# Kernel optimization log

Measured on AMD Instinct MI355X. Metric: run time of the kernel, lower is better.

## Reference

```python
import jax, jax.numpy as jnp
import numpy as np

B, S, C, H, W = 4, 8, 3, 384, 384
K = 5
CK = C * K


def conv1x1(x, w, b):
    # x: [B, Cin, H, W], w: [Cout, Cin], b: [Cout] -> [B, Cout, H, W]
    return jnp.einsum('bchw,oc->bohw', x, w) + b[None, :, None, None]


def mlp(x, w1, b1, w2, b2):
    return conv1x1(jax.nn.relu(conv1x1(x, w1, b1)), w2, b2)


def gaussian_density(x, mu_k, sigma):
    # x: [B,C,H,W], mu_k: [B,K,C,H,W], sigma: [B,K,H,W] -> density [B,K,H,W]
    s2 = sigma * sigma
    dist = jnp.sum((x[:, None] - mu_k) ** 2, axis=2)  # [B,K,H,W]
    return (2.0 * np.pi * s2) ** (-C / 2.0) * jnp.exp(-dist / (2.0 * s2))


def gmm_block(params, x, pi, mu, sigma):
    b = x.shape[0]
    mu_k = mu.reshape(b, K, C, H, W)
    dens = gaussian_density(x, mu_k, sigma)          # [B,K,H,W] (computed once, reused)
    alpha = pi * dens                                 # [B,K,H,W]
    rho = alpha * dens                                # [B,K,H,W]
    pi_new = jax.nn.softmax(mlp(jnp.concatenate([pi, alpha], 1), *params['pi']), axis=1)
    mu_new = jax.nn.sigmoid(mlp(jnp.concatenate([x, mu, rho], 1), *params['mu']))
    sigma_new = jnp.exp(jax.nn.relu(mlp(jnp.concatenate([x, mu_new, rho], 1), *params['sigma'])))
    dens2 = gaussian_density(x, mu_new.reshape(b, K, C, H, W), sigma_new)
    gamma = jax.nn.sigmoid(mlp(pi_new * dens2, *params['gamma']))  # [B,1,H,W]
    return pi_new, mu_new, sigma_new, gamma


def setup_inputs() -> dict:
    key = jax.random.key(0)
    ks = jax.random.split(key, 20)
    frames = jax.random.uniform(ks[0], (B, S, C, H, W), jnp.float32)
    targets = jax.random.uniform(ks[1], (B, S, C, H, W), jnp.float32)
    mu0 = jax.random.randint(ks[2], (B, CK, H, W), 0, 255).astype(jnp.float32) / 255.0
    def wb(k1, k2, cout, cin):
        return (jax.random.normal(k1, (cout, cin), jnp.float32) * 0.1,
                jax.random.normal(k2, (cout,), jnp.float32) * 0.1)
    pi_w1, pi_b1 = wb(ks[3], ks[4], K, 2 * K)
    pi_w2, pi_b2 = wb(ks[5], ks[6], K, K)
    mu_w1, mu_b1 = wb(ks[7], ks[8], CK, C + CK + K)
    mu_w2, mu_b2 = wb(ks[9], ks[10], CK, CK)
    sg_w1, sg_b1 = wb(ks[11], ks[12], K, C + CK + K)
    sg_w2, sg_b2 = wb(ks[13], ks[14], K, K)
    ga_w1, ga_b1 = wb(ks[15], ks[16], K, K)
    ga_w2, ga_b2 = wb(ks[17], ks[18], 1, K)
    return dict(frames=frames, targets=targets, mu0=mu0,
                pi_w1=pi_w1, pi_b1=pi_b1, pi_w2=pi_w2, pi_b2=pi_b2,
                mu_w1=mu_w1, mu_b1=mu_b1, mu_w2=mu_w2, mu_b2=mu_b2,
                sg_w1=sg_w1, sg_b1=sg_b1, sg_w2=sg_w2, sg_b2=sg_b2,
                ga_w1=ga_w1, ga_b1=ga_b1, ga_w2=ga_w2, ga_b2=ga_b2)


def reference(frames, targets, mu0,
              pi_w1, pi_b1, pi_w2, pi_b2,
              mu_w1, mu_b1, mu_w2, mu_b2,
              sg_w1, sg_b1, sg_w2, sg_b2,
              ga_w1, ga_b1, ga_w2, ga_b2):
    params = dict(pi=(pi_w1, pi_b1, pi_w2, pi_b2),
                  mu=(mu_w1, mu_b1, mu_w2, mu_b2),
                  sigma=(sg_w1, sg_b1, sg_w2, sg_b2),
                  gamma=(ga_w1, ga_b1, ga_w2, ga_b2))
    b = frames.shape[0]
    # init_gmm
    pi0 = jnp.ones((b, K, H, W), frames.dtype) / K
    sigma0 = jnp.ones((b, K, H, W), frames.dtype)

    def step(carry, frame):
        pi, mu, sigma = carry
        pi, mu, sigma, gamma = gmm_block(params, frame, pi, mu, sigma)
        return (pi, mu, sigma), gamma

    xs = jnp.moveaxis(frames, 1, 0)  # [S,B,C,H,W]
    _, gammas = jax.lax.scan(step, (pi0, mu0, sigma0), xs)
    return jnp.moveaxis(gammas, 0, 1)  # [B,S,1,H,W]
```

## Files before the change

### kernel.cpp

```cpp
#include <hip/hip_runtime.h>


namespace {

constexpr int Kk = 5;
constexpr int Cc = 3;
constexpr int CKc = 15;
constexpr int Bb = 4;
constexpr int Ss = 8;
constexpr int HWc = 384 * 384;
constexpr int BLOCK = 256;

constexpr int OPB1 = 0;
constexpr int OPW1 = 5;
constexpr int OPB2 = 55;
constexpr int OPW2 = 60;
constexpr int OMB1 = 85;
constexpr int OMW1 = 100;
constexpr int OMB2 = 445;
constexpr int OMW2 = 460;
constexpr int OSB1 = 685;
constexpr int OSW1 = 690;
constexpr int OSB2 = 805;
constexpr int OSW2 = 810;
constexpr int OGB1 = 835;
constexpr int OGW1 = 840;
constexpr int OGW2 = 865;
constexpr int OGB2 = 870;
constexpr int WTOT = 871;

__device__ __forceinline__ float rcpf(float x) { return __builtin_amdgcn_rcpf(x); }
__device__ __forceinline__ float ex2(float x) { return __builtin_amdgcn_exp2f(x); }
__device__ __forceinline__ float frelu(float a) { return fmaxf(a, 0.0f); }
constexpr float LOG2E = 1.4426950408889634f;
__device__ __forceinline__ float fsigm(float a) { return rcpf(1.0f + ex2(-LOG2E * a)); }

__global__ __launch_bounds__(256) void stage_ws_kernel(
    const float* __restrict__ pw1, const float* __restrict__ pb1,
    const float* __restrict__ pw2, const float* __restrict__ pb2,
    const float* __restrict__ mw1, const float* __restrict__ mb1,
    const float* __restrict__ mw2, const float* __restrict__ mb2,
    const float* __restrict__ sw1, const float* __restrict__ sb1,
    const float* __restrict__ sw2, const float* __restrict__ sb2,
    const float* __restrict__ gw1, const float* __restrict__ gb1,
    const float* __restrict__ gw2, const float* __restrict__ gb2,
    float* __restrict__ ws)
{
    const int t = threadIdx.x;
    auto cp = [&](const float* src, int off, int n) {
        for (int i = t; i < n; i += 256) ws[off + i] = src[i];
    };
    cp(pb1, OPB1, 5);   cp(pw1, OPW1, 50);
    cp(pb2, OPB2, 5);   cp(pw2, OPW2, 25);
    cp(mb1, OMB1, 15);  cp(mw1, OMW1, 345);
    cp(mb2, OMB2, 15);  cp(mw2, OMW2, 225);
    cp(sb1, OSB1, 5);   cp(sw1, OSW1, 115);
    cp(sb2, OSB2, 5);   cp(sw2, OSW2, 25);
    cp(gb1, OGB1, 5);   cp(gw1, OGW1, 25);
    cp(gw2, OGW2, 5);   cp(gb2, OGB2, 1);
}

__global__ __launch_bounds__(BLOCK, 4) void gmm_seq_kernel(
    const float* __restrict__ frames,
    const float* __restrict__ mu0,
    const float* __restrict__ Wt,
    float* __restrict__ out)
{
    const int t = blockIdx.x * BLOCK + threadIdx.x;
    const int b   = t / HWc;
    const int rem = t - b * HWc;

    const float C0 = 0.06349363593424097f;
    const float NH_L2E = -0.7213475204444817f;

    float pi[Kk], mu[CKc], rinv[Kk];
#pragma unroll
    for (int k = 0; k < Kk; k++) { pi[k] = 0.2f; rinv[k] = 1.0f; }
    {
        const float* mp = mu0 + (size_t)b * CKc * HWc;
#pragma unroll
        for (int j = 0; j < CKc; j++)
            mu[j] = mp[(size_t)j * HWc + rem];
    }

    const float* fbase = frames + ((size_t)b * Ss * Cc) * HWc;
    float x[Cc];
#pragma unroll
    for (int c = 0; c < Cc; c++)
        x[c] = fbase[(size_t)c * HWc + rem];

#pragma unroll 1
    for (int s = 0; s < Ss; s++) {
        long woff = 0;
        asm volatile("" : "+s"(woff));
        const float* W = Wt + woff;

        const int sn = (s + 1 < Ss) ? s + 1 : s;
        float xn[Cc];
        {
            const float* fp = fbase + ((size_t)sn * Cc) * HWc;
#pragma unroll
            for (int c = 0; c < Cc; c++)
                xn[c] = fp[(size_t)c * HWc + rem];
        }

        float alpha[Kk], rho[Kk];
#pragma unroll
        for (int k = 0; k < Kk; k++) {
            float inv_s2 = rinv[k] * rinv[k];
            float d0 = x[0] - mu[k * Cc + 0];
            float d1 = x[1] - mu[k * Cc + 1];
            float d2 = x[2] - mu[k * Cc + 2];
            float dist = fmaf(d0, d0, fmaf(d1, d1, d2 * d2));
            float coef = C0 * inv_s2 * rinv[k];
            float dens = coef * ex2(NH_L2E * dist * inv_s2);
            alpha[k] = pi[k] * dens;
            rho[k] = alpha[k] * dens;
        }

        float piN[Kk];
        {
            float h[Kk];
#pragma unroll
            for (int j = 0; j < Kk; j++) {
                float a = W[OPB1 + j];
#pragma unroll
                for (int i = 0; i < Kk; i++) a = fmaf(W[OPW1 + j * 2 * Kk + i], pi[i], a);
#pragma unroll
                for (int i = 0; i < Kk; i++) a = fmaf(W[OPW1 + j * 2 * Kk + Kk + i], alpha[i], a);
                h[j] = frelu(a);
            }
            float o[Kk];
            float m = -1e30f;
#pragma unroll
            for (int j = 0; j < Kk; j++) {
                float a = W[OPB2 + j];
#pragma unroll
                for (int i = 0; i < Kk; i++) a = fmaf(W[OPW2 + j * Kk + i], h[i], a);
                o[j] = a; m = fmaxf(m, a);
            }
            float sum = 0.0f;
#pragma unroll
            for (int j = 0; j < Kk; j++) { o[j] = ex2(LOG2E * (o[j] - m)); sum += o[j]; }
            float r = rcpf(sum);
#pragma unroll
            for (int j = 0; j < Kk; j++) piN[j] = o[j] * r;
        }

        float muN[CKc];
        {
            float h[CKc];
#pragma unroll
            for (int j = 0; j < CKc; j++) {
                float a = W[OMB1 + j];
#pragma unroll
                for (int i = 0; i < Cc; i++)  a = fmaf(W[OMW1 + j * 23 + i], x[i], a);
#pragma unroll
                for (int i = 0; i < CKc; i++) a = fmaf(W[OMW1 + j * 23 + 3 + i], mu[i], a);
#pragma unroll
                for (int i = 0; i < Kk; i++)  a = fmaf(W[OMW1 + j * 23 + 18 + i], rho[i], a);
                h[j] = frelu(a);
            }
#pragma unroll
            for (int j = 0; j < CKc; j++) {
                float a = W[OMB2 + j];
#pragma unroll
                for (int i = 0; i < CKc; i++) a = fmaf(W[OMW2 + j * CKc + i], h[i], a);
                muN[j] = fsigm(a);
            }
        }

        float rinvN[Kk];
        {
            float h[Kk];
#pragma unroll
            for (int j = 0; j < Kk; j++) {
                float a = W[OSB1 + j];
#pragma unroll
                for (int i = 0; i < Cc; i++)  a = fmaf(W[OSW1 + j * 23 + i], x[i], a);
#pragma unroll
                for (int i = 0; i < CKc; i++) a = fmaf(W[OSW1 + j * 23 + 3 + i], muN[i], a);
#pragma unroll
                for (int i = 0; i < Kk; i++)  a = fmaf(W[OSW1 + j * 23 + 18 + i], rho[i], a);
                h[j] = frelu(a);
            }
#pragma unroll
            for (int j = 0; j < Kk; j++) {
                float a = W[OSB2 + j];
#pragma unroll
                for (int i = 0; i < Kk; i++) a = fmaf(W[OSW2 + j * Kk + i], h[i], a);
                rinvN[j] = ex2(-LOG2E * frelu(a));
            }
        }

        float gin[Kk];
#pragma unroll
        for (int k = 0; k < Kk; k++) {
            float inv_s2 = rinvN[k] * rinvN[k];
            float d0 = x[0] - muN[k * Cc + 0];
            float d1 = x[1] - muN[k * Cc + 1];
            float d2 = x[2] - muN[k * Cc + 2];
            float dist = fmaf(d0, d0, fmaf(d1, d1, d2 * d2));
            float coef = C0 * inv_s2 * rinvN[k];
            gin[k] = piN[k] * (coef * ex2(NH_L2E * dist * inv_s2));
        }
        {
            float h[Kk];
#pragma unroll
            for (int j = 0; j < Kk; j++) {
                float a = W[OGB1 + j];
#pragma unroll
                for (int i = 0; i < Kk; i++) a = fmaf(W[OGW1 + j * Kk + i], gin[i], a);
                h[j] = frelu(a);
            }
            float go = W[OGB2];
#pragma unroll
            for (int i = 0; i < Kk; i++) go = fmaf(W[OGW2 + i], h[i], go);
            out[(size_t)(b * Ss + s) * HWc + rem] = fsigm(go);
        }

#pragma unroll
        for (int k = 0; k < Kk; k++) { pi[k] = piN[k]; rinv[k] = rinvN[k]; }
#pragma unroll
        for (int j = 0; j < CKc; j++) mu[j] = muN[j];
#pragma unroll
        for (int c = 0; c < Cc; c++) x[c] = xn[c];
    }
}

}

extern "C" void kernel_launch(void* const* d_in, const int* in_sizes, int n_in,
                              void* d_out, int out_size, void* d_ws, size_t ws_size,
                              hipStream_t stream) {
    const float* frames = (const float*)d_in[0];
    const float* mu0    = (const float*)d_in[2];
    const float* pw1 = (const float*)d_in[3];
    const float* pb1 = (const float*)d_in[4];
    const float* pw2 = (const float*)d_in[5];
    const float* pb2 = (const float*)d_in[6];
    const float* mw1 = (const float*)d_in[7];
    const float* mb1 = (const float*)d_in[8];
    const float* mw2 = (const float*)d_in[9];
    const float* mb2 = (const float*)d_in[10];
    const float* sw1 = (const float*)d_in[11];
    const float* sb1 = (const float*)d_in[12];
    const float* sw2 = (const float*)d_in[13];
    const float* sb2 = (const float*)d_in[14];
    const float* gw1 = (const float*)d_in[15];
    const float* gb1 = (const float*)d_in[16];
    const float* gw2 = (const float*)d_in[17];
    const float* gb2 = (const float*)d_in[18];
    float* out = (float*)d_out;
    float* ws  = (float*)d_ws;

    stage_ws_kernel<<<1, 256, 0, stream>>>(
        pw1, pb1, pw2, pb2, mw1, mb1, mw2, mb2,
        sw1, sb1, sw2, sb2, gw1, gb1, gw2, gb2, ws);

    const int total = Bb * HWc;
    const int grid = (total + BLOCK - 1) / BLOCK;

    gmm_seq_kernel<<<grid, BLOCK, 0, stream>>>(frames, mu0, ws, out);
}
```

Before: 302.5 us.

## Pack MLP outputs into float2 pairs for packed FMA on CDNA

```diff
diff --git a/kernel.cpp b/kernel.cpp
--- a/kernel.cpp
+++ b/kernel.cpp
@@ -3,37 +3,59 @@
 
 namespace {
 
-constexpr int Kk = 5;
 constexpr int Cc = 3;
-constexpr int CKc = 15;
 constexpr int Bb = 4;
 constexpr int Ss = 8;
 constexpr int HWc = 384 * 384;
 constexpr int BLOCK = 256;
 
 constexpr int OPB1 = 0;
-constexpr int OPW1 = 5;
-constexpr int OPB2 = 55;
-constexpr int OPW2 = 60;
-constexpr int OMB1 = 85;
-constexpr int OMW1 = 100;
-constexpr int OMB2 = 445;
-constexpr int OMW2 = 460;
-constexpr int OSB1 = 685;
-constexpr int OSW1 = 690;
-constexpr int OSB2 = 805;
-constexpr int OSW2 = 810;
-constexpr int OGB1 = 835;
-constexpr int OGW1 = 840;
-constexpr int OGW2 = 865;
-constexpr int OGB2 = 870;
-constexpr int WTOT = 871;
+constexpr int OPW1 = 6;
+constexpr int OPB2 = 66;
+constexpr int OPW2 = 72;
+constexpr int OMB1 = 102;
+constexpr int OMW1 = 118;
+constexpr int OMB2 = 486;
+constexpr int OMW2 = 504;
+constexpr int OSB1 = 774;
+constexpr int OSW1 = 780;
+constexpr int OSB2 = 918;
+constexpr int OSW2 = 924;
+constexpr int OGB1 = 954;
+constexpr int OGW1 = 960;
+constexpr int OGW2 = 990;
+constexpr int OGB2 = 995;
+constexpr int WTOT = 996;
+
+constexpr int HPB1 = OPB1 / 2;
+constexpr int HPW1 = OPW1 / 2;
+constexpr int HPB2 = OPB2 / 2;
+constexpr int HPW2 = OPW2 / 2;
+constexpr int HMB1 = OMB1 / 2;
+constexpr int HMW1 = OMW1 / 2;
+constexpr int HMB2 = OMB2 / 2;
+constexpr int HMW2 = OMW2 / 2;
+constexpr int HSB1 = OSB1 / 2;
+constexpr int HSW1 = OSW1 / 2;
+constexpr int HSB2 = OSB2 / 2;
+constexpr int HSW2 = OSW2 / 2;
+constexpr int HGB1 = OGB1 / 2;
+constexpr int HGW1 = OGW1 / 2;
+
+typedef float v2f __attribute__((ext_vector_type(2)));
 
 __device__ __forceinline__ float rcpf(float x) { return __builtin_amdgcn_rcpf(x); }
 __device__ __forceinline__ float ex2(float x) { return __builtin_amdgcn_exp2f(x); }
-__device__ __forceinline__ float frelu(float a) { return fmaxf(a, 0.0f); }
+
+__device__ __forceinline__ v2f vsplat(float w) { v2f r = {w, w}; return r; }
+__device__ __forceinline__ v2f vfma(v2f a, v2f b, v2f c) { return __builtin_elementwise_fma(a, b, c); }
+__device__ __forceinline__ v2f vexp2(v2f v) { v2f r; r.x = ex2(v.x); r.y = ex2(v.y); return r; }
+__device__ __forceinline__ v2f vrcp(v2f v) { v2f r; r.x = rcpf(v.x); r.y = rcpf(v.y); return r; }
+__device__ __forceinline__ v2f vmax(v2f a, v2f b) { return __builtin_elementwise_max(a, b); }
+__device__ __forceinline__ v2f vrelu(v2f a) { return vmax(a, vsplat(0.0f)); }
 constexpr float LOG2E = 1.4426950408889634f;
-__device__ __forceinline__ float fsigm(float a) { return rcpf(1.0f + ex2(-LOG2E * a)); }
+__device__ __forceinline__ v2f vsigm(v2f a) { return vrcp(vsplat(1.0f) + vexp2(vsplat(-LOG2E) * a)); }
+__device__ __forceinline__ float hx(v2f v, int sel) { return sel ? v.y : v.x; }
 
 __global__ __launch_bounds__(256) void stage_ws_kernel(
     const float* __restrict__ pw1, const float* __restrict__ pb1,
@@ -47,20 +69,34 @@
     float* __restrict__ ws)
 {
     const int t = threadIdx.x;
-    auto cp = [&](const float* src, int off, int n) {
-        for (int i = t; i < n; i += 256) ws[off + i] = src[i];
+    auto pairs = [&](const float* w, const float* bsrc, int I, int NP,
+                     const int* lo, const int* hi, int wOff, int bOff) {
+        for (int idx = t; idx < I * NP; idx += 256) {
+            int i = idx / NP, p = idx - (idx / NP) * NP;
+            ws[wOff + 2 * idx]     = w[lo[p] * I + i];
+            ws[wOff + 2 * idx + 1] = (hi[p] >= 0) ? w[hi[p] * I + i] : 0.0f;
+        }
+        for (int p = t; p < NP; p += 256) {
+            ws[bOff + 2 * p]     = bsrc[lo[p]];
+            ws[bOff + 2 * p + 1] = (hi[p] >= 0) ? bsrc[hi[p]] : 0.0f;
+        }
     };
-    cp(pb1, OPB1, 5);   cp(pw1, OPW1, 50);
-    cp(pb2, OPB2, 5);   cp(pw2, OPW2, 25);
-    cp(mb1, OMB1, 15);  cp(mw1, OMW1, 345);
-    cp(mb2, OMB2, 15);  cp(mw2, OMW2, 225);
-    cp(sb1, OSB1, 5);   cp(sw1, OSW1, 115);
-    cp(sb2, OSB2, 5);   cp(sw2, OSW2, 25);
-    cp(gb1, OGB1, 5);   cp(gw1, OGW1, 25);
-    cp(gw2, OGW2, 5);   cp(gb2, OGB2, 1);
+    const int lo3[3] = {0, 2, 4},                 hi3[3] = {1, 3, -1};
+    const int lo8[8] = {0, 2, 4, 6, 8, 10, 12, 14}, hi8[8] = {1, 3, 5, 7, 9, 11, 13, -1};
+    const int lo9[9] = {0, 1, 2, 6, 7, 8, 12, 13, 14}, hi9[9] = {3, 4, 5, 9, 10, 11, -1, -1, -1};
+    pairs(pw1, pb1, 10, 3, lo3, hi3, OPW1, OPB1);
+    pairs(pw2, pb2,  5, 3, lo3, hi3, OPW2, OPB2);
+    pairs(mw1, mb1, 23, 8, lo8, hi8, OMW1, OMB1);
+    pairs(mw2, mb2, 15, 9, lo9, hi9, OMW2, OMB2);
+    pairs(sw1, sb1, 23, 3, lo3, hi3, OSW1, OSB1);
+    pairs(sw2, sb2,  5, 3, lo3, hi3, OSW2, OSB2);
+    pairs(gw1, gb1,  5, 3, lo3, hi3, OGW1, OGB1);
+    if (t < 5)  ws[OGW2 + t] = gw2[t];
+    if (t == 0) ws[OGB2] = gb2[0];
 }
 
-__global__ __launch_bounds__(BLOCK, 4) void gmm_seq_kernel(
+__global__ __launch_bounds__(BLOCK, 4)
+void gmm_seq_kernel(
     const float* __restrict__ frames,
     const float* __restrict__ mu0,
     const float* __restrict__ Wt,
@@ -73,156 +109,205 @@
     const float C0 = 0.06349363593424097f;
     const float NH_L2E = -0.7213475204444817f;
 
-    float pi[Kk], mu[CKc], rinv[Kk];
-#pragma unroll
-    for (int k = 0; k < Kk; k++) { pi[k] = 0.2f; rinv[k] = 1.0f; }
+    v2f piP[3], muP[9], rinvP[3];
+    piP[0] = vsplat(0.2f); piP[1] = vsplat(0.2f); piP[2] = {0.2f, 0.0f};
+    rinvP[0] = vsplat(1.0f); rinvP[1] = vsplat(1.0f); rinvP[2] = {1.0f, 0.0f};
     {
-        const float* mp = mu0 + (size_t)b * CKc * HWc;
-#pragma unroll
-        for (int j = 0; j < CKc; j++)
-            mu[j] = mp[(size_t)j * HWc + rem];
+        const float* mp = mu0 + (size_t)b * 15 * HWc;
+#pragma unroll
+        for (int kp = 0; kp < 3; kp++)
+#pragma unroll
+            for (int c = 0; c < 3; c++) {
+                float lo = mp[(size_t)((2 * kp) * 3 + c) * HWc + rem];
+                float hi = (kp < 2) ? mp[(size_t)((2 * kp + 1) * 3 + c) * HWc + rem] : 0.0f;
+                muP[kp * 3 + c] = {lo, hi};
+            }
     }
 
     const float* fbase = frames + ((size_t)b * Ss * Cc) * HWc;
     float x[Cc];
 #pragma unroll
-    for (int c = 0; c < Cc; c++)
-        x[c] = fbase[(size_t)c * HWc + rem];
+    for (int c = 0; c < Cc; c++) x[c] = fbase[(size_t)c * HWc + rem];
 
 #pragma unroll 1
     for (int s = 0; s < Ss; s++) {
         long woff = 0;
         asm volatile("" : "+s"(woff));
         const float* W = Wt + woff;
+        const v2f* W2 = reinterpret_cast<const v2f*>(W);
 
         const int sn = (s + 1 < Ss) ? s + 1 : s;
         float xn[Cc];
         {
             const float* fp = fbase + ((size_t)sn * Cc) * HWc;
 #pragma unroll
-            for (int c = 0; c < Cc; c++)
-                xn[c] = fp[(size_t)c * HWc + rem];
-        }
-
-        float alpha[Kk], rho[Kk];
-#pragma unroll
-        for (int k = 0; k < Kk; k++) {
-            float inv_s2 = rinv[k] * rinv[k];
-            float d0 = x[0] - mu[k * Cc + 0];
-            float d1 = x[1] - mu[k * Cc + 1];
-            float d2 = x[2] - mu[k * Cc + 2];
-            float dist = fmaf(d0, d0, fmaf(d1, d1, d2 * d2));
-            float coef = C0 * inv_s2 * rinv[k];
-            float dens = coef * ex2(NH_L2E * dist * inv_s2);
-            alpha[k] = pi[k] * dens;
-            rho[k] = alpha[k] * dens;
-        }
-
-        float piN[Kk];
-        {
-            float h[Kk];
-#pragma unroll
-            for (int j = 0; j < Kk; j++) {
-                float a = W[OPB1 + j];
-#pragma unroll
-                for (int i = 0; i < Kk; i++) a = fmaf(W[OPW1 + j * 2 * Kk + i], pi[i], a);
-#pragma unroll
-                for (int i = 0; i < Kk; i++) a = fmaf(W[OPW1 + j * 2 * Kk + Kk + i], alpha[i], a);
-                h[j] = frelu(a);
-            }
-            float o[Kk];
-            float m = -1e30f;
-#pragma unroll
-            for (int j = 0; j < Kk; j++) {
-                float a = W[OPB2 + j];
-#pragma unroll
-                for (int i = 0; i < Kk; i++) a = fmaf(W[OPW2 + j * Kk + i], h[i], a);
-                o[j] = a; m = fmaxf(m, a);
-            }
-            float sum = 0.0f;
-#pragma unroll
-            for (int j = 0; j < Kk; j++) { o[j] = ex2(LOG2E * (o[j] - m)); sum += o[j]; }
+            for (int c = 0; c < Cc; c++) xn[c] = fp[(size_t)c * HWc + rem];
+        }
+
+        v2f xs[Cc];
+#pragma unroll
+        for (int c = 0; c < Cc; c++) xs[c] = vsplat(x[c]);
+
+        v2f alpha2[3], rho2[3];
+#pragma unroll
+        for (int kp = 0; kp < 3; kp++) {
+            v2f ri  = rinvP[kp];
+            v2f is2 = ri * ri;
+            v2f d0 = xs[0] - muP[kp * 3 + 0];
+            v2f d1 = xs[1] - muP[kp * 3 + 1];
+            v2f d2 = xs[2] - muP[kp * 3 + 2];
+            v2f dist = vfma(d0, d0, vfma(d1, d1, d2 * d2));
+            v2f coef = vsplat(C0) * is2 * ri;
+            v2f dens = coef * vexp2(vsplat(NH_L2E) * dist * is2);
+            alpha2[kp] = piP[kp] * dens;
+            rho2[kp]   = alpha2[kp] * dens;
+        }
+
+        {
+            v2f hp[3];
+#pragma unroll
+            for (int p = 0; p < 3; p++) hp[p] = W2[HPB1 + p];
+#pragma unroll
+            for (int i = 0; i < 5; i++) {
+                v2f sv = vsplat(hx(piP[i >> 1], i & 1));
+#pragma unroll
+                for (int p = 0; p < 3; p++) hp[p] = vfma(W2[HPW1 + i * 3 + p], sv, hp[p]);
+            }
+#pragma unroll
+            for (int i = 0; i < 5; i++) {
+                v2f sv = vsplat(hx(alpha2[i >> 1], i & 1));
+#pragma unroll
+                for (int p = 0; p < 3; p++) hp[p] = vfma(W2[HPW1 + (5 + i) * 3 + p], sv, hp[p]);
+            }
+#pragma unroll
+            for (int p = 0; p < 3; p++) hp[p] = vrelu(hp[p]);
+
+            v2f o2[3];
+#pragma unroll
+            for (int p = 0; p < 3; p++) o2[p] = W2[HPB2 + p];
+#pragma unroll
+            for (int i = 0; i < 5; i++) {
+                v2f sv = vsplat(hx(hp[i >> 1], i & 1));
+#pragma unroll
+                for (int p = 0; p < 3; p++) o2[p] = vfma(W2[HPW2 + i * 3 + p], sv, o2[p]);
+            }
+            float m = fmaxf(fmaxf(fmaxf(o2[0].x, o2[0].y), fmaxf(o2[1].x, o2[1].y)), o2[2].x);
+            v2f e0 = vexp2(vsplat(LOG2E) * (o2[0] - vsplat(m)));
+            v2f e1 = vexp2(vsplat(LOG2E) * (o2[1] - vsplat(m)));
+            v2f e2 = vexp2(vsplat(LOG2E) * (o2[2] - vsplat(m)));
+            float sum = e0.x + e0.y + e1.x + e1.y + e2.x;
             float r = rcpf(sum);
-#pragma unroll
-            for (int j = 0; j < Kk; j++) piN[j] = o[j] * r;
-        }
-
-        float muN[CKc];
-        {
-            float h[CKc];
-#pragma unroll
-            for (int j = 0; j < CKc; j++) {
-                float a = W[OMB1 + j];
-#pragma unroll
-                for (int i = 0; i < Cc; i++)  a = fmaf(W[OMW1 + j * 23 + i], x[i], a);
-#pragma unroll
-                for (int i = 0; i < CKc; i++) a = fmaf(W[OMW1 + j * 23 + 3 + i], mu[i], a);
-#pragma unroll
-                for (int i = 0; i < Kk; i++)  a = fmaf(W[OMW1 + j * 23 + 18 + i], rho[i], a);
-                h[j] = frelu(a);
-            }
-#pragma unroll
-            for (int j = 0; j < CKc; j++) {
-                float a = W[OMB2 + j];
-#pragma unroll
-                for (int i = 0; i < CKc; i++) a = fmaf(W[OMW2 + j * CKc + i], h[i], a);
-                muN[j] = fsigm(a);
-            }
-        }
-
-        float rinvN[Kk];
-        {
-            float h[Kk];
-#pragma unroll
-            for (int j = 0; j < Kk; j++) {
-                float a = W[OSB1 + j];
-#pragma unroll
-                for (int i = 0; i < Cc; i++)  a = fmaf(W[OSW1 + j * 23 + i], x[i], a);
-#pragma unroll
-                for (int i = 0; i < CKc; i++) a = fmaf(W[OSW1 + j * 23 + 3 + i], muN[i], a);
-#pragma unroll
-                for (int i = 0; i < Kk; i++)  a = fmaf(W[OSW1 + j * 23 + 18 + i], rho[i], a);
-                h[j] = frelu(a);
-            }
-#pragma unroll
-            for (int j = 0; j < Kk; j++) {
-                float a = W[OSB2 + j];
-#pragma unroll
-                for (int i = 0; i < Kk; i++) a = fmaf(W[OSW2 + j * Kk + i], h[i], a);
-                rinvN[j] = ex2(-LOG2E * frelu(a));
-            }
-        }
-
-        float gin[Kk];
-#pragma unroll
-        for (int k = 0; k < Kk; k++) {
-            float inv_s2 = rinvN[k] * rinvN[k];
-            float d0 = x[0] - muN[k * Cc + 0];
-            float d1 = x[1] - muN[k * Cc + 1];
-            float d2 = x[2] - muN[k * Cc + 2];
-            float dist = fmaf(d0, d0, fmaf(d1, d1, d2 * d2));
-            float coef = C0 * inv_s2 * rinvN[k];
-            gin[k] = piN[k] * (coef * ex2(NH_L2E * dist * inv_s2));
-        }
-        {
-            float h[Kk];
-#pragma unroll
-            for (int j = 0; j < Kk; j++) {
-                float a = W[OGB1 + j];
-#pragma unroll
-                for (int i = 0; i < Kk; i++) a = fmaf(W[OGW1 + j * Kk + i], gin[i], a);
-                h[j] = frelu(a);
-            }
+            piP[0] = e0 * vsplat(r); piP[1] = e1 * vsplat(r); piP[2] = e2 * vsplat(r);
+        }
+
+        {
+            v2f hm[8];
+#pragma unroll
+            for (int p = 0; p < 8; p++) hm[p] = W2[HMB1 + p];
+#pragma unroll
+            for (int c = 0; c < 3; c++) {
+#pragma unroll
+                for (int p = 0; p < 8; p++) hm[p] = vfma(W2[HMW1 + c * 8 + p], xs[c], hm[p]);
+            }
+#pragma unroll
+            for (int j = 0; j < 15; j++) {
+                const int k = j / 3, c = j - 3 * (j / 3);
+                v2f sv = vsplat(hx(muP[(k >> 1) * 3 + c], k & 1));
+#pragma unroll
+                for (int p = 0; p < 8; p++) hm[p] = vfma(W2[HMW1 + (3 + j) * 8 + p], sv, hm[p]);
+            }
+#pragma unroll
+            for (int k = 0; k < 5; k++) {
+                v2f sv = vsplat(hx(rho2[k >> 1], k & 1));
+#pragma unroll
+                for (int p = 0; p < 8; p++) hm[p] = vfma(W2[HMW1 + (18 + k) * 8 + p], sv, hm[p]);
+            }
+#pragma unroll
+            for (int p = 0; p < 8; p++) hm[p] = vrelu(hm[p]);
+
+            v2f am[9];
+#pragma unroll
+            for (int q = 0; q < 9; q++) am[q] = W2[HMB2 + q];
+#pragma unroll
+            for (int j = 0; j < 15; j++) {
+                v2f sv = vsplat(hx(hm[j >> 1], j & 1));
+#pragma unroll
+                for (int q = 0; q < 9; q++) am[q] = vfma(W2[HMW2 + j * 9 + q], sv, am[q]);
+            }
+#pragma unroll
+            for (int q = 0; q < 9; q++) muP[q] = vsigm(am[q]);
+        }
+
+        {
+            v2f hs[3];
+#pragma unroll
+            for (int p = 0; p < 3; p++) hs[p] = W2[HSB1 + p];
+#pragma unroll
+            for (int c = 0; c < 3; c++) {
+#pragma unroll
+                for (int p = 0; p < 3; p++) hs[p] = vfma(W2[HSW1 + c * 3 + p], xs[c], hs[p]);
+            }
+#pragma unroll
+            for (int j = 0; j < 15; j++) {
+                const int k = j / 3, c = j - 3 * (j / 3);
+                v2f sv = vsplat(hx(muP[(k >> 1) * 3 + c], k & 1));
+#pragma unroll
+                for (int p = 0; p < 3; p++) hs[p] = vfma(W2[HSW1 + (3 + j) * 3 + p], sv, hs[p]);
+            }
+#pragma unroll
+            for (int k = 0; k < 5; k++) {
+                v2f sv = vsplat(hx(rho2[k >> 1], k & 1));
+#pragma unroll
+                for (int p = 0; p < 3; p++) hs[p] = vfma(W2[HSW1 + (18 + k) * 3 + p], sv, hs[p]);
+            }
+#pragma unroll
+            for (int p = 0; p < 3; p++) hs[p] = vrelu(hs[p]);
+
+            v2f as2[3];
+#pragma unroll
+            for (int p = 0; p < 3; p++) as2[p] = W2[HSB2 + p];
+#pragma unroll
+            for (int i = 0; i < 5; i++) {
+                v2f sv = vsplat(hx(hs[i >> 1], i & 1));
+#pragma unroll
+                for (int p = 0; p < 3; p++) as2[p] = vfma(W2[HSW2 + i * 3 + p], sv, as2[p]);
+            }
+#pragma unroll
+            for (int p = 0; p < 3; p++)
+                rinvP[p] = vexp2(vsplat(-LOG2E) * vrelu(as2[p]));
+        }
+
+        v2f gin[3];
+#pragma unroll
+        for (int kp = 0; kp < 3; kp++) {
+            v2f ri  = rinvP[kp];
+            v2f is2 = ri * ri;
+            v2f d0 = xs[0] - muP[kp * 3 + 0];
+            v2f d1 = xs[1] - muP[kp * 3 + 1];
+            v2f d2 = xs[2] - muP[kp * 3 + 2];
+            v2f dist = vfma(d0, d0, vfma(d1, d1, d2 * d2));
+            v2f coef = vsplat(C0) * is2 * ri;
+            gin[kp] = piP[kp] * (coef * vexp2(vsplat(NH_L2E) * dist * is2));
+        }
+        {
+            v2f hg[3];
+#pragma unroll
+            for (int p = 0; p < 3; p++) hg[p] = W2[HGB1 + p];
+#pragma unroll
+            for (int i = 0; i < 5; i++) {
+                v2f sv = vsplat(hx(gin[i >> 1], i & 1));
+#pragma unroll
+                for (int p = 0; p < 3; p++) hg[p] = vfma(W2[HGW1 + i * 3 + p], sv, hg[p]);
+            }
+#pragma unroll
+            for (int p = 0; p < 3; p++) hg[p] = vrelu(hg[p]);
+
             float go = W[OGB2];
 #pragma unroll
-            for (int i = 0; i < Kk; i++) go = fmaf(W[OGW2 + i], h[i], go);
-            out[(size_t)(b * Ss + s) * HWc + rem] = fsigm(go);
-        }
-
-#pragma unroll
-        for (int k = 0; k < Kk; k++) { pi[k] = piN[k]; rinv[k] = rinvN[k]; }
-#pragma unroll
-        for (int j = 0; j < CKc; j++) mu[j] = muN[j];
+            for (int i = 0; i < 5; i++) go = fmaf(W[OGW2 + i], hx(hg[i >> 1], i & 1), go);
+            out[(size_t)(b * Ss + s) * HWc + rem] = rcpf(1.0f + ex2(-LOG2E * go));
+        }
+
 #pragma unroll
         for (int c = 0; c < Cc; c++) x[c] = xn[c];
     }
```

Measured after the change: 282.0 us. -6.8%, faster.
